# Optimization experiments

Hardware: AMD Instinct MI355X
Metric: run time of the kernel (lower is better)

The kernel has to match this reference:

```python
import jax, jax.numpy as jnp
import numpy as np

D_MODEL = 256
H, W = 48, 48
BATCH = 16


def setup_inputs() -> dict:
    key = jax.random.key(0)
    ks = jax.random.split(key, 8)
    s = 1.0 / np.sqrt(D_MODEL)
    return {
        "x": jax.random.normal(ks[0], (BATCH, H, W, D_MODEL), jnp.float32),
        "wq": jax.random.normal(ks[1], (D_MODEL, D_MODEL), jnp.float32) * s,
        "bq": jnp.zeros((D_MODEL,), jnp.float32),
        "wk": jax.random.normal(ks[2], (D_MODEL, D_MODEL), jnp.float32) * s,
        "bk": jnp.zeros((D_MODEL,), jnp.float32),
        "wv": jax.random.normal(ks[3], (D_MODEL, D_MODEL), jnp.float32) * s,
        "bv": jnp.zeros((D_MODEL,), jnp.float32),
        "pos_emb": jax.random.normal(ks[4], (H * W, D_MODEL), jnp.float32) * 0.02,
    }


def reference(x, wq, bq, wk, bk, wv, bv, pos_emb):
    B, Hy, Wx, C = x.shape  # C == d_model
    # positional embedding added before QKV projections
    x = x + pos_emb.reshape(Hy, Wx, C)
    q = (x @ wq + bq).reshape(B, Hy * Wx, C)  # [B, S, d]
    k = (x @ wk + bk).reshape(B, Hy * Wx, C)
    v = (x @ wv + bv).reshape(B, Hy * Wx, C)
    scale = 1.0 / jnp.sqrt(jnp.asarray(C, jnp.float32))
    logits = jnp.einsum("bqd,bkd->bqk", q, k) * scale  # [B, S, S]
    attn = jax.nn.softmax(logits, axis=-1)
    out = jnp.einsum("bqk,bkd->bqd", attn, v)  # [B, S, d]
    return out.reshape(B, Hy, Wx, C)
```

## Files before the change

kernel.cpp:

```cpp
#include <hip/hip_runtime.h>

typedef __attribute__((ext_vector_type(4))) float f32x4;
typedef __attribute__((ext_vector_type(8))) short bf16x8;
typedef __attribute__((ext_vector_type(4))) int i32x4;
typedef __attribute__((ext_vector_type(2))) unsigned int u32x2;

#define SCL2 0.09016844f

__device__ __forceinline__ unsigned short f2bf(float f) {
    unsigned int u = __float_as_uint(f);
    u = (u + 0x7FFFu + ((u >> 16) & 1u)) >> 16;
    return (unsigned short)u;
}

__device__ __forceinline__ f32x4 mfma16(bf16x8 a, bf16x8 b, f32x4 c) {
    return __builtin_amdgcn_mfma_f32_16x16x32_bf16(a, b, c, 0, 0, 0);
}

__device__ __forceinline__ unsigned cvtpk(float lo, float hi) {
    unsigned r;
    asm("v_cvt_pk_bf16_f32 %0, %1, %2" : "=v"(r) : "v"(lo), "v"(hi));
    return r;
}

__device__ __forceinline__ void pl32swap(unsigned &a, unsigned &b) {
#if __has_builtin(__builtin_amdgcn_permlane32_swap)
    u32x2 r = __builtin_amdgcn_permlane32_swap(a, b, false, false);
    a = r[0]; b = r[1];
#else
    asm volatile("v_permlane32_swap_b32 %0, %1" : "+v"(a), "+&v"(b));
#endif
}
__device__ __forceinline__ void pl16swap(unsigned &a, unsigned &b) {
#if __has_builtin(__builtin_amdgcn_permlane16_swap)
    u32x2 r = __builtin_amdgcn_permlane16_swap(a, b, false, false);
    a = r[0]; b = r[1];
#else
    asm volatile("v_permlane16_swap_b32 %0, %1" : "+v"(a), "+&v"(b));
#endif
}

__device__ __forceinline__ float redmax4(float x) {
    unsigned a = __float_as_uint(x), b = a;
    pl32swap(a, b);
    x = fmaxf(__uint_as_float(a), __uint_as_float(b));
    a = __float_as_uint(x); b = a;
    pl16swap(a, b);
    return fmaxf(__uint_as_float(a), __uint_as_float(b));
}
__device__ __forceinline__ float redsum4(float x) {
    unsigned a = __float_as_uint(x), b = a;
    pl32swap(a, b);
    x = __uint_as_float(a) + __uint_as_float(b);
    a = __float_as_uint(x); b = a;
    pl16swap(a, b);
    return __uint_as_float(a) + __uint_as_float(b);
}

__global__ void prep_x(const float* __restrict__ x, const float* __restrict__ pos,
                       unsigned short* __restrict__ xb) {
    int t = blockIdx.x * 256 + threadIdx.x;
    int e = t * 8;
    int row  = e >> 8;
    int prow = row % 2304;
    int col  = e & 255;
    const float4* xp = (const float4*)(x + e);
    const float4* pp = (const float4*)(pos + prow * 256 + col);
    float4 a0 = xp[0], a1 = xp[1];
    float4 p0 = pp[0], p1 = pp[1];
    bf16x8 o;
    o[0] = (short)f2bf(a0.x + p0.x);  o[1] = (short)f2bf(a0.y + p0.y);
    o[2] = (short)f2bf(a0.z + p0.z);  o[3] = (short)f2bf(a0.w + p0.w);
    o[4] = (short)f2bf(a1.x + p1.x);  o[5] = (short)f2bf(a1.y + p1.y);
    o[6] = (short)f2bf(a1.z + p1.z);  o[7] = (short)f2bf(a1.w + p1.w);
    *(bf16x8*)(xb + e) = o;
}

__global__ void prep_w(const float* __restrict__ wq, const float* __restrict__ wk,
                       const float* __restrict__ wv, const float* __restrict__ bq,
                       const float* __restrict__ bk, const float* __restrict__ bv,
                       unsigned short* __restrict__ wT, float* __restrict__ bias) {
    int t = blockIdx.x * 256 + threadIdx.x;
    int n = t >> 8, k = t & 255;
    const float* w = (n < 256) ? wq : (n < 512) ? wk : wv;
    int col = n & 255;
    wT[t] = f2bf(w[k * 256 + col]);
    if (t < 768) {
        const float* bs = (t < 256) ? bq : (t < 512) ? bk : bv;
        bias[t] = bs[t & 255];
    }
}

__global__ __launch_bounds__(256)
void qkv_gemm(const unsigned short* __restrict__ xb,
              const unsigned short* __restrict__ wT,
              const float* __restrict__ bias,
              unsigned short* __restrict__ qb,
              unsigned short* __restrict__ kb,
              unsigned short* __restrict__ vtb) {
    __shared__ __align__(16) char Al[16384];
    __shared__ __align__(16) char Bl[16384];
    int rm0 = blockIdx.y * 128;
    int bn0 = blockIdx.x * 128;
    int tid = threadIdx.x;
    int lane = tid & 63, w = tid >> 6;
    int wr = w >> 1, wc = w & 1;
    int l15 = lane & 15, l4 = lane >> 4;

    int soff[4];
    {
        int h = lane >> 3, s8 = lane & 7;
        #pragma unroll
        for (int i = 0; i < 4; ++i) {
            int lr = w * 32 + i * 8 + h;
            soff[i] = lr * 512 + ((s8 * 16) ^ ((lr & 7) << 4));
        }
    }
    const char* aB = (const char*)xb + (size_t)rm0 * 512;
    const char* bB = (const char*)wT + (size_t)bn0 * 512;

    f32x4 acc[4][4] = {};
    for (int k0 = 0; k0 < 256; k0 += 64) {
        __syncthreads();
        #pragma unroll
        for (int i = 0; i < 4; ++i) {
            __builtin_amdgcn_global_load_lds(
                (const __attribute__((address_space(1))) unsigned int*)(aB + k0 * 2 + soff[i]),
                (__attribute__((address_space(3))) unsigned int*)(Al + w * 4096 + i * 1024),
                16, 0, 0);
            __builtin_amdgcn_global_load_lds(
                (const __attribute__((address_space(1))) unsigned int*)(bB + k0 * 2 + soff[i]),
                (__attribute__((address_space(3))) unsigned int*)(Bl + w * 4096 + i * 1024),
                16, 0, 0);
        }
        __syncthreads();
        #pragma unroll
        for (int kk = 0; kk < 2; ++kk) {
            bf16x8 af[4], bfr[4];
            #pragma unroll
            for (int mb = 0; mb < 4; ++mb) {
                int ar = wr * 64 + mb * 16 + l15;
                af[mb] = *(const bf16x8*)(Al + ar * 128 +
                          ((kk * 64 + l4 * 16) ^ ((ar & 7) << 4)));
            }
            #pragma unroll
            for (int nb = 0; nb < 4; ++nb) {
                int br = wc * 64 + nb * 16 + l15;
                bfr[nb] = *(const bf16x8*)(Bl + br * 128 +
                           ((kk * 64 + l4 * 16) ^ ((br & 7) << 4)));
            }
            #pragma unroll
            for (int mb = 0; mb < 4; ++mb)
                #pragma unroll
                for (int nb = 0; nb < 4; ++nb)
                    acc[mb][nb] = mfma16(af[mb], bfr[nb], acc[mb][nb]);
        }
    }
    int bidx = rm0 / 2304;
    #pragma unroll
    for (int mb = 0; mb < 4; ++mb) {
        int grow0 = rm0 + wr * 64 + mb * 16 + l4 * 4;
        int srow0 = grow0 - bidx * 2304;
        #pragma unroll
        for (int nb = 0; nb < 4; ++nb) {
            int n = bn0 + wc * 64 + nb * 16 + l15;
            float bs = bias[n];
            unsigned short h0 = f2bf(acc[mb][nb][0] + bs);
            unsigned short h1 = f2bf(acc[mb][nb][1] + bs);
            unsigned short h2 = f2bf(acc[mb][nb][2] + bs);
            unsigned short h3 = f2bf(acc[mb][nb][3] + bs);
            if (n < 256) {
                qb[(long)(grow0 + 0) * 256 + n] = h0;
                qb[(long)(grow0 + 1) * 256 + n] = h1;
                qb[(long)(grow0 + 2) * 256 + n] = h2;
                qb[(long)(grow0 + 3) * 256 + n] = h3;
            } else if (n < 512) {
                int nn = n - 256;
                kb[(long)(grow0 + 0) * 256 + nn] = h0;
                kb[(long)(grow0 + 1) * 256 + nn] = h1;
                kb[(long)(grow0 + 2) * 256 + nn] = h2;
                kb[(long)(grow0 + 3) * 256 + nn] = h3;
            } else {
                ushort4 pk4;
                pk4.x = h0; pk4.y = h1; pk4.z = h2; pk4.w = h3;
                *(ushort4*)(vtb + ((long)bidx * 256 + (n - 512)) * 2304 + srow0) = pk4;
            }
        }
    }
}

__global__ __launch_bounds__(256, 2)
void attn(const unsigned short* __restrict__ qb,
          const unsigned short* __restrict__ kbuf,
          const unsigned short* __restrict__ vtb,
          float* __restrict__ out) {
    __shared__ __align__(16) char lds[65536];

    int orig = blockIdx.x;
    int L = (orig & 7) * 72 + (orig >> 3);
    int b = L / 36, q0 = (L % 36) * 64;

    int tid = threadIdx.x;
    int lane = tid & 63, w = tid >> 6;
    int l15 = lane & 15, l4 = lane >> 4;

    const char* kgB = (const char*)(kbuf + (size_t)b * 2304 * 256);
    const unsigned short* vgB = vtb + (size_t)b * 256 * 2304;

    int koff[4], voff[4];
    {
        int h = lane >> 5, slot = lane & 31;
        #pragma unroll
        for (int i = 0; i < 4; ++i) {
            int lr = w * 8 + i * 2 + h;
            koff[i] = lr * 512 + ((slot * 16) ^ ((lr & 7) << 4));
        }
        int s4 = lane & 3;
        #pragma unroll
        for (int i = 0; i < 4; ++i) {
            int dr = w * 64 + i * 16 + (lane >> 2);
            int g = s4 ^ ((dr >> 1) & 3);
            voff[i] = dr * 2304 + g * 8;
        }
    }

    auto stage = [&](int kv0, int buf) {
        char* kdst = lds + buf * 16384 + w * 4096;
        const char* ksrc = kgB + (size_t)kv0 * 512;
        #pragma unroll
        for (int i = 0; i < 4; ++i)
            __builtin_amdgcn_global_load_lds(
                (const __attribute__((address_space(1))) unsigned int*)(ksrc + koff[i]),
                (__attribute__((address_space(3))) unsigned int*)(kdst + i * 1024),
                16, 0, 0);
        char* vdst = lds + 32768 + buf * 16384 + w * 4096;
        #pragma unroll
        for (int i = 0; i < 4; ++i)
            __builtin_amdgcn_global_load_lds(
                (const __attribute__((address_space(1))) unsigned int*)(vgB + kv0 + voff[i]),
                (__attribute__((address_space(3))) unsigned int*)(vdst + i * 1024),
                16, 0, 0);
    };

    stage(0, 0);

    bf16x8 qf[8];
    {
        const unsigned short* qrow = qb + ((size_t)b * 2304 + q0 + w * 16 + l15) * 256;
        #pragma unroll
        for (int kbk = 0; kbk < 8; ++kbk)
            qf[kbk] = *(const bf16x8*)(qrow + kbk * 32 + l4 * 8);
    }

    f32x4 o[16] = {};
    float m = -__builtin_inff(), l = 0.f;
    int vslot = (l4 ^ ((l15 >> 1) & 3)) * 16;

    for (int t = 0; t < 72; ++t) {
        __syncthreads();
        if (t < 71) stage((t + 1) * 32, (t + 1) & 1);

        const char* kl = lds + (t & 1) * 16384;
        f32x4 s[2] = {};
        #pragma unroll
        for (int kbk = 0; kbk < 8; ++kbk) {
            #pragma unroll
            for (int cb = 0; cb < 2; ++cb) {
                int row = cb * 16 + l15;
                bf16x8 kf = *(const bf16x8*)(kl + row * 512 +
                             ((kbk * 64 + l4 * 16) ^ ((row & 7) << 4)));
                s[cb] = mfma16(kf, qf[kbk], s[cb]);
            }
        }

        float p[8];
        #pragma unroll
        for (int cb = 0; cb < 2; ++cb)
            #pragma unroll
            for (int j = 0; j < 4; ++j)
                p[cb * 4 + j] = s[cb][j] * SCL2;
        float mx = fmaxf(fmaxf(fmaxf(p[0], p[1]), fmaxf(p[2], p[3])),
                         fmaxf(fmaxf(p[4], p[5]), fmaxf(p[6], p[7])));
        mx = redmax4(mx);
        if (__any(mx > m + 8.f)) {
            float mn = fmaxf(m, mx);
            float alpha = exp2f(m - mn);
            float aj[4];
            #pragma unroll
            for (int j = 0; j < 4; ++j) aj[j] = __shfl(alpha, l4 * 4 + j);
            #pragma unroll
            for (int nb = 0; nb < 16; ++nb)
                #pragma unroll
                for (int j = 0; j < 4; ++j) o[nb][j] *= aj[j];
            l *= alpha;
            m = mn;
        }
        float rs = 0.f;
        #pragma unroll
        for (int i = 0; i < 8; ++i) { p[i] = exp2f(p[i] - m); rs += p[i]; }
        l += redsum4(rs);

        unsigned c0 = cvtpk(p[0], p[1]);
        unsigned c1 = cvtpk(p[2], p[3]);
        unsigned c2 = cvtpk(p[4], p[5]);
        unsigned c3 = cvtpk(p[6], p[7]);
        pl32swap(c0, c2);
        pl32swap(c1, c3);
        pl16swap(c0, c2);
        pl16swap(c1, c3);
        i32x4 pw; pw[0] = (int)c0; pw[1] = (int)c1; pw[2] = (int)c2; pw[3] = (int)c3;
        bf16x8 pf = *(bf16x8*)&pw;

        const char* vl = lds + 32768 + (t & 1) * 16384;
        #pragma unroll
        for (int nb = 0; nb < 16; ++nb) {
            bf16x8 vf = *(const bf16x8*)(vl + (nb * 16 + l15) * 64 + vslot);
            o[nb] = mfma16(pf, vf, o[nb]);
        }
    }

    float linv[4];
    #pragma unroll
    for (int j = 0; j < 4; ++j) linv[j] = 1.0f / __shfl(l, l4 * 4 + j);
    size_t obase = ((size_t)b * 2304 + q0 + w * 16) * 256;
    #pragma unroll
    for (int nb = 0; nb < 16; ++nb)
        #pragma unroll
        for (int j = 0; j < 4; ++j)
            out[obase + (size_t)(l4 * 4 + j) * 256 + nb * 16 + l15] = o[nb][j] * linv[j];
}

extern "C" void kernel_launch(void* const* d_in, const int* in_sizes, int n_in,
                              void* d_out, int out_size, void* d_ws, size_t ws_size,
                              hipStream_t stream) {
    const float* x   = (const float*)d_in[0];
    const float* wq  = (const float*)d_in[1];
    const float* bq  = (const float*)d_in[2];
    const float* wk  = (const float*)d_in[3];
    const float* bk  = (const float*)d_in[4];
    const float* wv  = (const float*)d_in[5];
    const float* bv  = (const float*)d_in[6];
    const float* pos = (const float*)d_in[7];

    const long NROW = 36864;
    unsigned short* xb  = (unsigned short*)d_ws;
    unsigned short* qbf = xb  + NROW * 256;
    unsigned short* kbf = qbf + NROW * 256;
    unsigned short* vtb = kbf + NROW * 256;
    unsigned short* wT  = vtb + NROW * 256;
    float* bias = (float*)(wT + 768 * 256);

    prep_x<<<4608, 256, 0, stream>>>(x, pos, xb);
    prep_w<<<768, 256, 0, stream>>>(wq, wk, wv, bq, bk, bv, wT, bias);
    qkv_gemm<<<dim3(6, 288), 256, 0, stream>>>(xb, wT, bias, qbf, kbf, vtb);
    attn<<<576, 256, 0, stream>>>(qbf, kbf, vtb, (float*)d_out);
}
```

Before: 292.0 us.

## Split attention KV range in halves and process two query tiles per wave

Each attention block now handles 128 queries (two 16-row tiles per wave that share each K/V fragment load from LDS) over half of the key sequence. Unnormalised partial outputs and their max/sum statistics are written out, and a new combine kernel merges the two halves. This raises MFMA work per LDS read and keeps the same grid size, at the cost of more registers, an extra fp32 partial-output round trip through memory, and an additional kernel launch. The exp2 calls also switch to the hardware intrinsic.

```diff
diff --git a/kernel.cpp b/kernel.cpp
--- a/kernel.cpp
+++ b/kernel.cpp
@@ -55,6 +55,43 @@
     a = __float_as_uint(x); b = a;
     pl16swap(a, b);
     return __uint_as_float(a) + __uint_as_float(b);
+}
+
+__device__ __forceinline__ bf16x8 softmax_pack(const f32x4 (&s)[2], float &m, float &l,
+                                               f32x4 (&o)[16], int l4) {
+    float p[8];
+    #pragma unroll
+    for (int cb = 0; cb < 2; ++cb)
+        #pragma unroll
+        for (int j = 0; j < 4; ++j)
+            p[cb * 4 + j] = s[cb][j] * SCL2;
+    float mx = fmaxf(fmaxf(fmaxf(p[0], p[1]), fmaxf(p[2], p[3])),
+                     fmaxf(fmaxf(p[4], p[5]), fmaxf(p[6], p[7])));
+    mx = redmax4(mx);
+    if (__any(mx > m + 8.f)) {
+        float mn = fmaxf(m, mx);
+        float alpha = __builtin_amdgcn_exp2f(m - mn);
+        float aj[4];
+        #pragma unroll
+        for (int j = 0; j < 4; ++j) aj[j] = __shfl(alpha, l4 * 4 + j);
+        #pragma unroll
+        for (int nb = 0; nb < 16; ++nb)
+            #pragma unroll
+            for (int j = 0; j < 4; ++j) o[nb][j] *= aj[j];
+        l *= alpha; m = mn;
+    }
+    float rs = 0.f;
+    #pragma unroll
+    for (int i = 0; i < 8; ++i) { p[i] = __builtin_amdgcn_exp2f(p[i] - m); rs += p[i]; }
+    l += redsum4(rs);
+    unsigned c0 = cvtpk(p[0], p[1]);
+    unsigned c1 = cvtpk(p[2], p[3]);
+    unsigned c2 = cvtpk(p[4], p[5]);
+    unsigned c3 = cvtpk(p[6], p[7]);
+    pl32swap(c0, c2); pl32swap(c1, c3);
+    pl16swap(c0, c2); pl16swap(c1, c3);
+    i32x4 pw; pw[0] = (int)c0; pw[1] = (int)c1; pw[2] = (int)c2; pw[3] = (int)c3;
+    return *(bf16x8*)&pw;
 }
 
 __global__ void prep_x(const float* __restrict__ x, const float* __restrict__ pos,
@@ -193,19 +230,23 @@
 void attn(const unsigned short* __restrict__ qb,
           const unsigned short* __restrict__ kbuf,
           const unsigned short* __restrict__ vtb,
-          float* __restrict__ out) {
+          float* __restrict__ po0, float* __restrict__ po1,
+          float2* __restrict__ ml) {
     __shared__ __align__(16) char lds[65536];
 
     int orig = blockIdx.x;
     int L = (orig & 7) * 72 + (orig >> 3);
-    int b = L / 36, q0 = (L % 36) * 64;
+    int b = L / 36;
+    int rem = L - b * 36;
+    int qt = rem >> 1, half = rem & 1;
+    int q0 = qt * 128;
 
     int tid = threadIdx.x;
     int lane = tid & 63, w = tid >> 6;
     int l15 = lane & 15, l4 = lane >> 4;
 
-    const char* kgB = (const char*)(kbuf + (size_t)b * 2304 * 256);
-    const unsigned short* vgB = vtb + (size_t)b * 256 * 2304;
+    const char* kgB = (const char*)kbuf + ((size_t)b * 2304 + half * 1152) * 512;
+    const unsigned short* vgB = vtb + (size_t)b * 256 * 2304 + half * 1152;
 
     int koff[4], voff[4];
     {
@@ -244,24 +285,28 @@
 
     stage(0, 0);
 
-    bf16x8 qf[8];
+    bf16x8 qfA[8], qfB[8];
     {
-        const unsigned short* qrow = qb + ((size_t)b * 2304 + q0 + w * 16 + l15) * 256;
-        #pragma unroll
-        for (int kbk = 0; kbk < 8; ++kbk)
-            qf[kbk] = *(const bf16x8*)(qrow + kbk * 32 + l4 * 8);
-    }
-
-    f32x4 o[16] = {};
-    float m = -__builtin_inff(), l = 0.f;
+        const unsigned short* qrowA = qb + ((size_t)b * 2304 + q0 + w * 32 + l15) * 256;
+        const unsigned short* qrowB = qrowA + 16 * 256;
+        #pragma unroll
+        for (int kbk = 0; kbk < 8; ++kbk) {
+            qfA[kbk] = *(const bf16x8*)(qrowA + kbk * 32 + l4 * 8);
+            qfB[kbk] = *(const bf16x8*)(qrowB + kbk * 32 + l4 * 8);
+        }
+    }
+
+    f32x4 oA[16] = {}, oB[16] = {};
+    float mA = -__builtin_inff(), lA = 0.f;
+    float mB = -__builtin_inff(), lB = 0.f;
     int vslot = (l4 ^ ((l15 >> 1) & 3)) * 16;
 
-    for (int t = 0; t < 72; ++t) {
+    for (int t = 0; t < 36; ++t) {
         __syncthreads();
-        if (t < 71) stage((t + 1) * 32, (t + 1) & 1);
+        if (t < 35) stage((t + 1) * 32, (t + 1) & 1);
 
         const char* kl = lds + (t & 1) * 16384;
-        f32x4 s[2] = {};
+        f32x4 sA[2] = {}, sB[2] = {};
         #pragma unroll
         for (int kbk = 0; kbk < 8; ++kbk) {
             #pragma unroll
@@ -269,65 +314,62 @@
                 int row = cb * 16 + l15;
                 bf16x8 kf = *(const bf16x8*)(kl + row * 512 +
                              ((kbk * 64 + l4 * 16) ^ ((row & 7) << 4)));
-                s[cb] = mfma16(kf, qf[kbk], s[cb]);
+                sA[cb] = mfma16(kf, qfA[kbk], sA[cb]);
+                sB[cb] = mfma16(kf, qfB[kbk], sB[cb]);
             }
         }
 
-        float p[8];
-        #pragma unroll
-        for (int cb = 0; cb < 2; ++cb)
-            #pragma unroll
-            for (int j = 0; j < 4; ++j)
-                p[cb * 4 + j] = s[cb][j] * SCL2;
-        float mx = fmaxf(fmaxf(fmaxf(p[0], p[1]), fmaxf(p[2], p[3])),
-                         fmaxf(fmaxf(p[4], p[5]), fmaxf(p[6], p[7])));
-        mx = redmax4(mx);
-        if (__any(mx > m + 8.f)) {
-            float mn = fmaxf(m, mx);
-            float alpha = exp2f(m - mn);
-            float aj[4];
-            #pragma unroll
-            for (int j = 0; j < 4; ++j) aj[j] = __shfl(alpha, l4 * 4 + j);
-            #pragma unroll
-            for (int nb = 0; nb < 16; ++nb)
-                #pragma unroll
-                for (int j = 0; j < 4; ++j) o[nb][j] *= aj[j];
-            l *= alpha;
-            m = mn;
-        }
-        float rs = 0.f;
-        #pragma unroll
-        for (int i = 0; i < 8; ++i) { p[i] = exp2f(p[i] - m); rs += p[i]; }
-        l += redsum4(rs);
-
-        unsigned c0 = cvtpk(p[0], p[1]);
-        unsigned c1 = cvtpk(p[2], p[3]);
-        unsigned c2 = cvtpk(p[4], p[5]);
-        unsigned c3 = cvtpk(p[6], p[7]);
-        pl32swap(c0, c2);
-        pl32swap(c1, c3);
-        pl16swap(c0, c2);
-        pl16swap(c1, c3);
-        i32x4 pw; pw[0] = (int)c0; pw[1] = (int)c1; pw[2] = (int)c2; pw[3] = (int)c3;
-        bf16x8 pf = *(bf16x8*)&pw;
+        bf16x8 pfA = softmax_pack(sA, mA, lA, oA, l4);
+        bf16x8 pfB = softmax_pack(sB, mB, lB, oB, l4);
 
         const char* vl = lds + 32768 + (t & 1) * 16384;
         #pragma unroll
         for (int nb = 0; nb < 16; ++nb) {
             bf16x8 vf = *(const bf16x8*)(vl + (nb * 16 + l15) * 64 + vslot);
-            o[nb] = mfma16(pf, vf, o[nb]);
-        }
-    }
-
-    float linv[4];
-    #pragma unroll
-    for (int j = 0; j < 4; ++j) linv[j] = 1.0f / __shfl(l, l4 * 4 + j);
-    size_t obase = ((size_t)b * 2304 + q0 + w * 16) * 256;
+            oA[nb] = mfma16(pfA, vf, oA[nb]);
+            oB[nb] = mfma16(pfB, vf, oB[nb]);
+        }
+    }
+
+    float* po = half ? po1 : po0;
+    size_t rowA = (size_t)b * 2304 + q0 + w * 32;
+    size_t pb = rowA * 256;
     #pragma unroll
     for (int nb = 0; nb < 16; ++nb)
         #pragma unroll
         for (int j = 0; j < 4; ++j)
-            out[obase + (size_t)(l4 * 4 + j) * 256 + nb * 16 + l15] = o[nb][j] * linv[j];
+            po[pb + (size_t)(l4 * 4 + j) * 256 + nb * 16 + l15] = oA[nb][j];
+    pb = (rowA + 16) * 256;
+    #pragma unroll
+    for (int nb = 0; nb < 16; ++nb)
+        #pragma unroll
+        for (int j = 0; j < 4; ++j)
+            po[pb + (size_t)(l4 * 4 + j) * 256 + nb * 16 + l15] = oB[nb][j];
+    if (l4 == 0) {
+        int mlbase = half * 36864 + (int)rowA;
+        ml[mlbase + l15]      = make_float2(mA, lA);
+        ml[mlbase + 16 + l15] = make_float2(mB, lB);
+    }
+}
+
+__global__ void combine(float* __restrict__ po0, const float* __restrict__ po1,
+                        const float2* __restrict__ ml) {
+    int t = blockIdx.x * 256 + threadIdx.x;
+    int q = t >> 5;
+    int d0 = (t & 31) * 8;
+    float2 h0 = ml[q], h1 = ml[36864 + q];
+    float mT = fmaxf(h0.x, h1.x);
+    float w0 = __builtin_amdgcn_exp2f(h0.x - mT);
+    float w1 = __builtin_amdgcn_exp2f(h1.x - mT);
+    float inv = 1.f / (w0 * h0.y + w1 * h1.y);
+    w0 *= inv; w1 *= inv;
+    size_t base = (size_t)q * 256 + d0;
+    f32x4 a0 = *(const f32x4*)(po0 + base);
+    f32x4 a1 = *(const f32x4*)(po0 + base + 4);
+    f32x4 b0 = *(const f32x4*)(po1 + base);
+    f32x4 b1 = *(const f32x4*)(po1 + base + 4);
+    *(f32x4*)(po0 + base)     = a0 * w0 + b0 * w1;
+    *(f32x4*)(po0 + base + 4) = a1 * w0 + b1 * w1;
 }
 
 extern "C" void kernel_launch(void* const* d_in, const int* in_sizes, int n_in,
@@ -343,15 +385,18 @@
     const float* pos = (const float*)d_in[7];
 
     const long NROW = 36864;
-    unsigned short* xb  = (unsigned short*)d_ws;
-    unsigned short* qbf = xb  + NROW * 256;
+    unsigned short* qbf = (unsigned short*)d_ws;
     unsigned short* kbf = qbf + NROW * 256;
     unsigned short* vtb = kbf + NROW * 256;
     unsigned short* wT  = vtb + NROW * 256;
     float* bias = (float*)(wT + 768 * 256);
+    unsigned short* xb  = (unsigned short*)(bias + 768);
+    float* po1 = (float*)xb;
+    float2* ml = (float2*)(po1 + NROW * 256);
 
     prep_x<<<4608, 256, 0, stream>>>(x, pos, xb);
     prep_w<<<768, 256, 0, stream>>>(wq, wk, wv, bq, bk, bv, wT, bias);
     qkv_gemm<<<dim3(6, 288), 256, 0, stream>>>(xb, wT, bias, qbf, kbf, vtb);
-    attn<<<576, 256, 0, stream>>>(qbf, kbf, vtb, (float*)d_out);
-}
+    attn<<<576, 256, 0, stream>>>(qbf, kbf, vtb, (float*)d_out, po1, ml);
+    combine<<<4608, 256, 0, stream>>>((float*)d_out, po1, ml);
+}
```

After: 288.4 us. No clear change (-1.2%).
